# Kernel tuning notes

Measured on AMD Instinct MI355X. Metric: run time of the kernel, lower is better.

Reference implementation:

```python
import jax, jax.numpy as jnp
import numpy as np

BETA = 2.0  # init kwarg beta


def _roi_map(roi_params, H, W):
    # roi_params: (N, K, 4) = (mu_x, mu_y, sigma_x, sigma_y) in [0, 1]
    dtype = roi_params.dtype
    gx = (jnp.arange(W, dtype=dtype) + 0.5) / W  # x-coords of grid columns
    gy = (jnp.arange(H, dtype=dtype) + 0.5) / H  # y-coords of grid rows
    mu_x, mu_y = roi_params[:, :, 0], roi_params[:, :, 1]
    sg_x, sg_y = roi_params[:, :, 2], roi_params[:, :, 3]
    # separable generalized-Gaussian log pdf along each axis
    log_x = -(jnp.abs(gx[None, None, :] - mu_x[:, :, None]) / sg_x[:, :, None]) ** BETA  # (N,K,W)
    log_y = -(jnp.abs(gy[None, None, :] - mu_y[:, :, None]) / sg_y[:, :, None]) ** BETA  # (N,K,H)
    scores = jnp.exp(log_y[:, :, :, None] + log_x[:, :, None, :])  # (N,K,H,W)
    mx = jnp.max(scores, axis=(2, 3), keepdims=True)
    return scores / (mx + 1e-12)  # max-normalized attention maps


def setup_inputs() -> dict:
    key = jax.random.key(0)
    k1, k2 = jax.random.split(key)
    x = jax.random.normal(k1, (16, 128, 128, 256), dtype=jnp.float32)
    roi_params = jax.random.uniform(k2, (16, 64, 4), dtype=jnp.float32)
    return {"x": x, "roi_params": roi_params}


def reference(x, roi_params):
    N, H, W, d = x.shape
    roi_map = _roi_map(roi_params, H, W)           # (N,K,H,W)
    flat_map = roi_map.reshape(N, -1, H * W)        # (N,K,HW)
    flat_feats = x.reshape(N, H * W, d)             # (N,HW,d)
    roi_features = jnp.einsum('nrf,nfd->nrd', flat_map, flat_feats) / (H * W)
    return roi_features, roi_params, roi_map
```

## Files before the change

### kernel.cpp

```cpp
#include <hip/hip_runtime.h>
#include <hip/hip_bf16.h>
#include <math.h>

#define NB 16
#define RB 64
#define HB 128
#define WB 128
#define DB 256
#define HW (HB * WB)

typedef __attribute__((ext_vector_type(8))) short bf16x8;
typedef __attribute__((ext_vector_type(4))) float f32x4;

static __device__ __forceinline__ short f2bf(float f) {
  __hip_bfloat16 h = __float2bfloat16(f);
  return *reinterpret_cast<short*>(&h);
}

#define GLOAD_LDS16(gp, lp)                                          \
  __builtin_amdgcn_global_load_lds(                                  \
      (const __attribute__((address_space(1))) unsigned int*)(gp),   \
      (__attribute__((address_space(3))) unsigned int*)(lp), 16, 0, 0)

__global__ void tables_kernel(const float* __restrict__ roi,
                              float* __restrict__ ws,
                              float* __restrict__ out_params) {
  const int nr = blockIdx.x;
  const int t  = threadIdx.x;

  const float mux = roi[nr * 4 + 0];
  const float muy = roi[nr * 4 + 1];
  const float sgx = roi[nr * 4 + 2];
  const float sgy = roi[nr * 4 + 3];

  const float g  = (t + 0.5f) * (1.0f / 128.0f);
  const float tx = fabsf(g - mux) / sgx;
  const float ty = fabsf(g - muy) / sgy;
  const float lx = -(tx * tx);
  const float ly = -(ty * ty);

  __shared__ float sdx[128], sdy[128];
  sdx[t] = lx; sdy[t] = ly;
  __syncthreads();
  for (int off = 64; off > 0; off >>= 1) {
    if (t < off) {
      sdx[t] = fmaxf(sdx[t], sdx[t + off]);
      sdy[t] = fmaxf(sdy[t], sdy[t + off]);
    }
    __syncthreads();
  }
  const float mlx = sdx[0], mly = sdy[0];

  const float em = expf(mlx + mly);
  const float s  = em / (em + 1e-12f);
  const float exv = expf(lx - mlx);
  const float eyv = expf(ly - mly) * s;

  float* ex_m = ws;
  float* ey_m = ws + NB * RB * WB;
  ex_m[nr * WB + t] = exv;
  ey_m[nr * HB + t] = eyv;

  if (t < 4) out_params[nr * 4 + t] = roi[nr * 4 + t];
}

__global__ void map_kernel(const float* __restrict__ ws,
                           float* __restrict__ out_map) {
  const float* ex_m = ws;
  const float* ey_m = ws + NB * RB * WB;
  const int total = NB * RB * HB * WB / 4;
  for (int idx = blockIdx.x * blockDim.x + threadIdx.x; idx < total;
       idx += gridDim.x * blockDim.x) {
    const int w4 = idx & 31;
    const int h  = (idx >> 5) & 127;
    const int nr = idx >> 12;
    const float  ey = ey_m[nr * HB + h];
    const float4 ex = *reinterpret_cast<const float4*>(ex_m + nr * WB + w4 * 4);
    float4 o;
    o.x = ey * ex.x; o.y = ey * ex.y; o.z = ey * ex.z; o.w = ey * ex.w;
    reinterpret_cast<float4*>(out_map)[idx] = o;
  }
}

__global__ __launch_bounds__(256, 1) void feat_mfma_kernel(
    const float* __restrict__ x, const float* __restrict__ ws,
    float* __restrict__ partials) {
  __shared__ float buf[4][32 * DB];

  const float* ex_m = ws;
  const float* ey_m = ws + NB * RB * WB;

  const int bid = blockIdx.x;
  const int n   = bid >> 5;
  const int kc  = bid & 31;
  const int t   = threadIdx.x;
  const int l   = t & 63;
  const int wv  = t >> 6;
  const int l15 = l & 15;
  const int lk  = (l >> 4) * 8;
  const int h0  = kc * 4;

  const char* gx =
      (const char*)(x + ((size_t)n * HW + (size_t)kc * 512) * DB);
  char* lbase = (char*)&buf[0][0];

  f32x4 exr[4][4][2];
  float eyv[4][4];
#pragma unroll
  for (int rf = 0; rf < 4; ++rf) {
    const float* exrow = ex_m + (size_t)(n * RB + rf * 16 + l15) * WB;
#pragma unroll
    for (int ks = 0; ks < 4; ++ks) {
      exr[rf][ks][0] = *reinterpret_cast<const f32x4*>(exrow + ks * 32 + lk);
      exr[rf][ks][1] = *reinterpret_cast<const f32x4*>(exrow + ks * 32 + lk + 4);
    }
  }
#pragma unroll
  for (int hh = 0; hh < 4; ++hh)
#pragma unroll
    for (int rf = 0; rf < 4; ++rf)
      eyv[hh][rf] = ey_m[(size_t)(n * RB + rf * 16 + l15) * HB + h0 + hh];
  asm volatile("s_waitcnt vmcnt(0)" ::: "memory");

  f32x4 acc[4][4];
#pragma unroll
  for (int rf = 0; rf < 4; ++rf)
#pragma unroll
    for (int f = 0; f < 4; ++f) acc[rf][f] = (f32x4)0.0f;

#define STAGE(bi, slot) do {                                                 \
    const char* gsrc_ = gx + (size_t)(bi) * 32768;                           \
    char* ldst_ = lbase + (slot) * 32768;                                    \
    _Pragma("unroll")                                                        \
    for (int ii = 0; ii < 8; ++ii)                                           \
      GLOAD_LDS16(gsrc_ + ii * 4096 + wv * 1024 + l * 16,                    \
                  ldst_ + ii * 4096 + wv * 1024);                            \
  } while (0)

  STAGE(0, 0); STAGE(1, 1); STAGE(2, 2);

#define KSTEP(bi, VM, DO_STAGE) do {                                         \
    asm volatile("s_waitcnt vmcnt(" #VM ")" ::: "memory");                   \
    __builtin_amdgcn_s_barrier();                                            \
    __builtin_amdgcn_sched_barrier(0);                                       \
    if (DO_STAGE) STAGE((bi) + 3, ((bi) + 3) & 3);                           \
    const float* bp_ = &buf[(bi) & 3][0];                                    \
    f32x4 xv_[8];                                                            \
    _Pragma("unroll")                                                        \
    for (int j = 0; j < 8; ++j)                                              \
      xv_[j] = *reinterpret_cast<const f32x4*>(                              \
          bp_ + (lk + j) * DB + wv * 64 + l15 * 4);                          \
    bf16x8 bfr_[4];                                                          \
    _Pragma("unroll")                                                        \
    for (int f = 0; f < 4; ++f) {                                            \
      bf16x8 b_;                                                             \
      _Pragma("unroll")                                                      \
      for (int j = 0; j < 8; ++j) b_[j] = f2bf(xv_[j][f]);                   \
      bfr_[f] = b_;                                                          \
    }                                                                        \
    bf16x8 afr_[4];                                                          \
    _Pragma("unroll")                                                        \
    for (int rf = 0; rf < 4; ++rf) {                                         \
      const float ey_ = eyv[(bi) >> 2][rf];                                  \
      const f32x4 e0_ = exr[rf][(bi) & 3][0];                                \
      const f32x4 e1_ = exr[rf][(bi) & 3][1];                                \
      bf16x8 a_;                                                             \
      a_[0] = f2bf(ey_ * e0_.x); a_[1] = f2bf(ey_ * e0_.y);                  \
      a_[2] = f2bf(ey_ * e0_.z); a_[3] = f2bf(ey_ * e0_.w);                  \
      a_[4] = f2bf(ey_ * e1_.x); a_[5] = f2bf(ey_ * e1_.y);                  \
      a_[6] = f2bf(ey_ * e1_.z); a_[7] = f2bf(ey_ * e1_.w);                  \
      afr_[rf] = a_;                                                         \
    }                                                                        \
    _Pragma("unroll")                                                        \
    for (int rf = 0; rf < 4; ++rf)                                           \
      _Pragma("unroll")                                                      \
      for (int f = 0; f < 4; ++f)                                            \
        acc[rf][f] = __builtin_amdgcn_mfma_f32_16x16x32_bf16(                \
            afr_[rf], bfr_[f], acc[rf][f], 0, 0, 0);                         \
  } while (0)

  KSTEP(0, 16, 1);  KSTEP(1, 16, 1);  KSTEP(2, 16, 1);  KSTEP(3, 16, 1);
  KSTEP(4, 16, 1);  KSTEP(5, 16, 1);  KSTEP(6, 16, 1);  KSTEP(7, 16, 1);
  KSTEP(8, 16, 1);  KSTEP(9, 16, 1);  KSTEP(10, 16, 1); KSTEP(11, 16, 1);
  KSTEP(12, 16, 1); KSTEP(13, 16, 0); KSTEP(14, 8, 0);  KSTEP(15, 0, 0);

#undef KSTEP
#undef STAGE

  float* P = partials + (size_t)bid * (RB * DB);
#pragma unroll
  for (int rf = 0; rf < 4; ++rf) {
#pragma unroll
    for (int reg = 0; reg < 4; ++reg) {
      const int r = rf * 16 + (l >> 4) * 4 + reg;
      f32x4 v;
      v.x = acc[rf][0][reg]; v.y = acc[rf][1][reg];
      v.z = acc[rf][2][reg]; v.w = acc[rf][3][reg];
      *reinterpret_cast<f32x4*>(P + (size_t)r * DB + wv * 64 + l15 * 4) = v;
    }
  }
}

__global__ __launch_bounds__(256) void reduce_kernel(
    const float* __restrict__ partials, float* __restrict__ outF) {
  const int idx = blockIdx.x * 256 + threadIdx.x;
  const int n   = idx >> 12;
  const int i4  = idx & 4095;
  const f32x4* p =
      reinterpret_cast<const f32x4*>(partials) + (size_t)n * 32 * 4096 + i4;
  f32x4 s0 = (f32x4)0.0f, s1 = (f32x4)0.0f, s2 = (f32x4)0.0f, s3 = (f32x4)0.0f;
#pragma unroll
  for (int kc = 0; kc < 32; kc += 4) {
    s0 += p[(size_t)(kc + 0) * 4096];
    s1 += p[(size_t)(kc + 1) * 4096];
    s2 += p[(size_t)(kc + 2) * 4096];
    s3 += p[(size_t)(kc + 3) * 4096];
  }
  f32x4 s = (s0 + s1) + (s2 + s3);
  s *= (1.0f / (float)HW);
  reinterpret_cast<f32x4*>(outF)[idx] = s;
}

extern "C" void kernel_launch(void* const* d_in, const int* in_sizes, int n_in,
                              void* d_out, int out_size, void* d_ws, size_t ws_size,
                              hipStream_t stream) {
  const float* x   = (const float*)d_in[0];
  const float* roi = (const float*)d_in[1];
  float* out        = (float*)d_out;
  float* ws         = (float*)d_ws;
  float* out_feat   = out;
  float* out_params = out + NB * RB * DB;
  float* out_map    = out_params + NB * RB * 4;

  float* P = out_map;

  tables_kernel<<<NB * RB, 128, 0, stream>>>(roi, ws, out_params);
  feat_mfma_kernel<<<512, 256, 0, stream>>>(x, ws, P);
  reduce_kernel<<<256, 256, 0, stream>>>(P, out_feat);
  map_kernel<<<2048, 256, 0, stream>>>(ws, out_map);
}
```

Measured before the change: 95.04 us.

## Fuse ROI map writes into feature MFMA kernel and move partials to workspace

```diff
diff --git a/kernel.cpp b/kernel.cpp
--- a/kernel.cpp
+++ b/kernel.cpp
@@ -82,9 +82,10 @@
   }
 }
 
+template <bool FUSE>
 __global__ __launch_bounds__(256, 1) void feat_mfma_kernel(
     const float* __restrict__ x, const float* __restrict__ ws,
-    float* __restrict__ partials) {
+    float* __restrict__ partials, float* __restrict__ out_map) {
   __shared__ float buf[4][32 * DB];
 
   const float* ex_m = ws;
@@ -120,6 +121,26 @@
 #pragma unroll
     for (int rf = 0; rf < 4; ++rf)
       eyv[hh][rf] = ey_m[(size_t)(n * RB + rf * 16 + l15) * HB + h0 + hh];
+
+  float eyw[4]; f32x4 exw[4][2];
+  float* mapW = nullptr;
+  if constexpr (FUSE) {
+    const int wvu = __builtin_amdgcn_readfirstlane(wv);
+#define SELW(RF) do {                                                        \
+      _Pragma("unroll")                                                      \
+      for (int hh = 0; hh < 4; ++hh) eyw[hh] = eyv[hh][RF];                  \
+      _Pragma("unroll")                                                      \
+      for (int ks = 0; ks < 4; ++ks) {                                       \
+        exw[ks][0] = exr[RF][ks][0]; exw[ks][1] = exr[RF][ks][1];            \
+      }                                                                      \
+    } while (0)
+    SELW(0);
+    if (wvu == 1) SELW(1);
+    else if (wvu == 2) SELW(2);
+    else if (wvu == 3) SELW(3);
+#undef SELW
+    mapW = out_map + (size_t)(n * RB + wv * 16 + l15) * HW + kc * 512 + lk;
+  }
   asm volatile("s_waitcnt vmcnt(0)" ::: "memory");
 
   f32x4 acc[4][4];
@@ -143,6 +164,13 @@
     asm volatile("s_waitcnt vmcnt(" #VM ")" ::: "memory");                   \
     __builtin_amdgcn_s_barrier();                                            \
     __builtin_amdgcn_sched_barrier(0);                                       \
+    if constexpr (FUSE) {                                                    \
+      const f32x4 eys_ = (f32x4)(eyw[(bi) >> 2]);                            \
+      *reinterpret_cast<f32x4*>(mapW + (bi) * 32)     =                      \
+          eys_ * exw[(bi) & 3][0];                                           \
+      *reinterpret_cast<f32x4*>(mapW + (bi) * 32 + 4) =                      \
+          eys_ * exw[(bi) & 3][1];                                           \
+    }                                                                        \
     if (DO_STAGE) STAGE((bi) + 3, ((bi) + 3) & 3);                           \
     const float* bp_ = &buf[(bi) & 3][0];                                    \
     f32x4 xv_[8];                                                            \
@@ -232,10 +260,20 @@
   float* out_params = out + NB * RB * DB;
   float* out_map    = out_params + NB * RB * 4;
 
-  float* P = out_map;
-
-  tables_kernel<<<NB * RB, 128, 0, stream>>>(roi, ws, out_params);
-  feat_mfma_kernel<<<512, 256, 0, stream>>>(x, ws, P);
-  reduce_kernel<<<256, 256, 0, stream>>>(P, out_feat);
-  map_kernel<<<2048, 256, 0, stream>>>(ws, out_map);
-}
+  const size_t tbl_floats = 2u * NB * RB * WB;
+  const size_t par_floats = 512u * RB * DB;
+  const bool ws_ok = ws_size >= (tbl_floats + par_floats + 16) * sizeof(float);
+
+  if (ws_ok) {
+    float* P = ws + tbl_floats;
+    tables_kernel<<<NB * RB, 128, 0, stream>>>(roi, ws, out_params);
+    feat_mfma_kernel<true><<<512, 256, 0, stream>>>(x, ws, P, out_map);
+    reduce_kernel<<<256, 256, 0, stream>>>(P, out_feat);
+  } else {
+    float* P = out_map;
+    tables_kernel<<<NB * RB, 128, 0, stream>>>(roi, ws, out_params);
+    feat_mfma_kernel<false><<<512, 256, 0, stream>>>(x, ws, P, out_map);
+    reduce_kernel<<<256, 256, 0, stream>>>(P, out_feat);
+    map_kernel<<<2048, 256, 0, stream>>>(ws, out_map);
+  }
+}
```

New measurement: 96.72 us. Within noise of the previous version (+1.8%).
